# Kernel optimization log

Measured on AMD Instinct MI355X. Metric: run time of the kernel, lower is better.

The kernel has to match this reference:

```python
import jax, jax.numpy as jnp
import numpy as np


def _gru_cell(x, h, W_ih, W_hh, b_ih, b_hh):
    # PyTorch GRUCell math, gate order (r, z, n) along the 3*H axis.
    gi = x @ W_ih.T + b_ih          # [B, 3H]
    gh = h @ W_hh.T + b_hh          # [B, 3H]
    i_r, i_z, i_n = jnp.split(gi, 3, axis=-1)
    h_r, h_z, h_n = jnp.split(gh, 3, axis=-1)
    r = jax.nn.sigmoid(i_r + h_r)
    z = jax.nn.sigmoid(i_z + h_z)
    n = jnp.tanh(i_n + r * h_n)
    return (1.0 - z) * n + z * h


def setup_inputs() -> dict:
    key = jax.random.key(0)
    ks = jax.random.split(key, 12)
    V, E, H, L, B, T = 16000, 512, 1024, 2, 32, 64
    s = 0.05  # small init scale to keep gates unsaturated
    return {
        "hidden": jax.random.normal(ks[0], (L, B, H), jnp.float32),
        "embed": jax.random.normal(ks[1], (V, E), jnp.float32) * s,
        "W_ih0": jax.random.normal(ks[2], (3 * H, E), jnp.float32) * s,
        "W_hh0": jax.random.normal(ks[3], (3 * H, H), jnp.float32) * s,
        "b_ih0": jax.random.normal(ks[4], (3 * H,), jnp.float32) * s,
        "b_hh0": jax.random.normal(ks[5], (3 * H,), jnp.float32) * s,
        "W_ih1": jax.random.normal(ks[6], (3 * H, H), jnp.float32) * s,
        "W_hh1": jax.random.normal(ks[7], (3 * H, H), jnp.float32) * s,
        "b_ih1": jax.random.normal(ks[8], (3 * H,), jnp.float32) * s,
        "b_hh1": jax.random.normal(ks[9], (3 * H,), jnp.float32) * s,
        "W_out": jax.random.normal(ks[10], (V, H), jnp.float32) * s,
        "b_out": jax.random.normal(ks[11], (V,), jnp.float32) * s,
        "max_len": 64,
        "batch_size": 32,
    }


def reference(hidden, embed, W_ih0, W_hh0, b_ih0, b_hh0,
              W_ih1, W_hh1, b_ih1, b_hh1, W_out, b_out,
              max_len, batch_size):
    # target=None path: teacher_forcing_ratio forced to 0 -> greedy argmax decode.
    tok0 = jnp.zeros((batch_size,), jnp.int32)  # curr_token starts at zeros

    def step(carry, _):
        h, tok = carry                      # h: [2, B, H], tok: [B] int32
        x = embed[tok]                      # [B, E] embedding lookup
        h0 = _gru_cell(x, h[0], W_ih0, W_hh0, b_ih0, b_hh0)
        h1 = _gru_cell(h0, h[1], W_ih1, W_hh1, b_ih1, b_hh1)
        logits = h1 @ W_out.T + b_out       # [B, V]
        tok_next = jnp.argmax(logits, axis=1).astype(jnp.int32)
        return (jnp.stack([h0, h1]), tok_next), logits

    (_, _), outputs = jax.lax.scan(step, (hidden, tok0), None, length=max_len)
    return outputs  # [max_len, B, V]
```

## Files before the change

### kernel.cpp

```cpp
#include <hip/hip_runtime.h>
#include <stdint.h>

#define V_ 16000
#define E_ 512
#define H_ 1024
#define B_ 32
#define T_ 64
#define NG_ 3072
#define NR_ 6144
#define IHB_ 96

typedef float f32x4 __attribute__((ext_vector_type(4)));
typedef unsigned long long u64;

__device__ __forceinline__ unsigned int fkey(float f) {
    unsigned int u = __float_as_uint(f);
    return (u & 0x80000000u) ? ~u : (u | 0x80000000u);
}

__global__ void init_kernel(const float* __restrict__ hidden,
                            float* __restrict__ h0, float* __restrict__ h1,
                            u64* __restrict__ tokpk) {
    int idx = blockIdx.x * blockDim.x + threadIdx.x;
    if (idx < B_ * H_) {
        h0[idx] = hidden[idx];
        h1[idx] = hidden[B_ * H_ + idx];
    }
    if (idx < T_ * B_) tokpk[idx] = 0ull;
}

__device__ __forceinline__ void gemm_core(
    const float* wp0, const float* wp1,
    const float* ap0, const float* ap1,
    int nch, float* lds, int tid, float acc[4][4])
{
    const int k4s = tid & 15;
    const int r   = tid >> 4;
    const int dW0 = (r << 6) + ((k4s ^ (r & 7)) << 2);
    const int dW1 = dW0 + (16 << 6);
    const int ks   = tid >> 6;
    const int lane = tid & 63;
    const int vg = lane >> 3, bg = lane & 7;

    f32x4 tW0, tW1, tA0, tA1;
    tW0 = *(const f32x4*)(wp0 + (k4s << 2));
    tW1 = *(const f32x4*)(wp1 + (k4s << 2));
    tA0 = *(const f32x4*)(ap0 + (k4s << 2));
    tA1 = *(const f32x4*)(ap1 + (k4s << 2));
    *(f32x4*)&lds[dW0] = tW0;        *(f32x4*)&lds[dW1] = tW1;
    *(f32x4*)&lds[2048 + dW0] = tA0; *(f32x4*)&lds[2048 + dW1] = tA1;
    __syncthreads();

    int cur = 0;
    for (int c = 0; c < nch; c++) {
        if (c + 1 < nch) {
            const int nko = (c + 1) << 6;
            tW0 = *(const f32x4*)(wp0 + nko + (k4s << 2));
            tW1 = *(const f32x4*)(wp1 + nko + (k4s << 2));
            tA0 = *(const f32x4*)(ap0 + nko + (k4s << 2));
            tA1 = *(const f32x4*)(ap1 + nko + (k4s << 2));
        }
        const float* Wb = &lds[cur * 4096];
        const float* Ab = &lds[cur * 4096 + 2048];
        #pragma unroll
        for (int kk = 0; kk < 4; kk++) {
            const int k4 = ks * 4 + kk;
            f32x4 ww[4], ha[4];
            #pragma unroll
            for (int vi = 0; vi < 4; vi++)
                ww[vi] = *(const f32x4*)&Wb[((vg + 8*vi) << 6) + ((k4 ^ vg) << 2)];
            #pragma unroll
            for (int j = 0; j < 4; j++)
                ha[j] = *(const f32x4*)&Ab[((bg + 8*j) << 6) + ((k4 ^ bg) << 2)];
            #pragma unroll
            for (int vi = 0; vi < 4; vi++)
                #pragma unroll
                for (int j = 0; j < 4; j++)
                    acc[vi][j] += ww[vi].x*ha[j].x + ww[vi].y*ha[j].y
                                + ww[vi].z*ha[j].z + ww[vi].w*ha[j].w;
        }
        if (c + 1 < nch) {
            float* Wo = &lds[(cur ^ 1) * 4096];
            *(f32x4*)&Wo[dW0] = tW0;        *(f32x4*)&Wo[dW1] = tW1;
            *(f32x4*)&Wo[2048 + dW0] = tA0; *(f32x4*)&Wo[2048 + dW1] = tA1;
        }
        __syncthreads();
        cur ^= 1;
    }
}

__device__ __forceinline__ void ks_reduce(float* lds, int tid,
                                          float acc[4][4], float tv[16])
{
    const int ks = tid >> 6, lane = tid & 63;
    float* red = lds;
    float* dst = &red[(ks * 64 + lane) * 17];
    #pragma unroll
    for (int vi = 0; vi < 4; vi++)
        #pragma unroll
        for (int j = 0; j < 4; j++) dst[vi*4 + j] = acc[vi][j];
    __syncthreads();
    if (tid < 64) {
        #pragma unroll
        for (int c = 0; c < 16; c++) {
            float s = 0.f;
            #pragma unroll
            for (int k = 0; k < 4; k++) s += red[(k*64 + tid)*17 + c];
            tv[c] = s;
        }
    }
}

__global__ __launch_bounds__(256) void gemm_gru(
    const float* __restrict__ Wih, const float* __restrict__ Whh, int Kih,
    const float* __restrict__ xbase, int xld,
    const float* __restrict__ embed, const u64* __restrict__ tokprev,
    int t, int tmode,
    const float* __restrict__ hprev,
    float* __restrict__ gbuf)
{
    __shared__ float lds[8192];
    const int tid = threadIdx.x;
    const int blk = blockIdx.x;
    const int r = tid >> 4;

    const float *wp0, *wp1, *ap0, *ap1;
    int nch;
    if (blk < IHB_) {
        const int n0 = blk * 32;
        wp0 = Wih + (size_t)(n0 + r) * Kih;
        wp1 = Wih + (size_t)(n0 + r + 16) * Kih;
        if (tmode) {
            int tok0 = 0, tok1 = 0;
            if (t > 0) {
                tok0 = (int)(0xFFFFFFFFu - (unsigned)(tokprev[r] & 0xFFFFFFFFull));
                tok1 = (int)(0xFFFFFFFFu - (unsigned)(tokprev[r + 16] & 0xFFFFFFFFull));
            }
            ap0 = embed + (size_t)tok0 * Kih;
            ap1 = embed + (size_t)tok1 * Kih;
        } else {
            ap0 = xbase + (size_t)r * xld;
            ap1 = xbase + (size_t)(r + 16) * xld;
        }
        nch = Kih >> 6;
    } else {
        const int n0 = (blk - IHB_) * 32;
        wp0 = Whh + (size_t)(n0 + r) * H_;
        wp1 = Whh + (size_t)(n0 + r + 16) * H_;
        ap0 = hprev + (size_t)r * H_;
        ap1 = hprev + (size_t)(r + 16) * H_;
        nch = H_ >> 6;
    }

    float acc[4][4] = {};
    gemm_core(wp0, wp1, ap0, ap1, nch, lds, tid, acc);
    float tv[16];
    ks_reduce(lds, tid, acc, tv);
    if (tid < 64) {
        const int vgr = tid >> 3, bgr = tid & 7;
        const int nout0 = blk * 32;
        #pragma unroll
        for (int vi = 0; vi < 4; vi++)
            #pragma unroll
            for (int j = 0; j < 4; j++)
                gbuf[(size_t)(bgr + 8*j) * NR_ + nout0 + vgr + 8*vi] = tv[vi*4+j];
    }
}

__global__ __launch_bounds__(256) void combine_kernel(
    const float* __restrict__ gbuf,
    const float* __restrict__ bih, const float* __restrict__ bhh,
    const float* __restrict__ hprev, float* __restrict__ hnew)
{
    const int idx = blockIdx.x * 256 + threadIdx.x;
    const int b = idx >> 10, i = idx & 1023;
    const float* gb = gbuf + (size_t)b * NR_;
    const float gir = gb[i],        giz = gb[H_ + i],        gin = gb[2*H_ + i];
    const float ghr = gb[NG_ + i],  ghz = gb[NG_ + H_ + i],  ghn = gb[NG_ + 2*H_ + i];
    const float Sr = gir + ghr + bih[i] + bhh[i];
    const float Sz = giz + ghz + bih[H_ + i] + bhh[H_ + i];
    const float rr = 1.f / (1.f + expf(-Sr));
    const float zz = 1.f / (1.f + expf(-Sz));
    const float nn = tanhf(gin + bih[2*H_ + i] + rr * (ghn + bhh[2*H_ + i]));
    const float hp = hprev[(size_t)b * H_ + i];
    hnew[(size_t)b * H_ + i] = (1.f - zz) * nn + zz * hp;
}

__global__ __launch_bounds__(256) void logits_kernel(
    const float* __restrict__ h1, const float* __restrict__ Wout,
    const float* __restrict__ bout, float* __restrict__ out_t,
    u64* __restrict__ tokpk_t)
{
    __shared__ float lds[8192];
    const int tid = threadIdx.x;
    const int r = tid >> 4;
    const int v0 = blockIdx.x * 32;
    const float* wp0 = Wout + (size_t)(v0 + r) * H_;
    const float* wp1 = Wout + (size_t)(v0 + r + 16) * H_;
    const float* ap0 = h1 + (size_t)r * H_;
    const float* ap1 = h1 + (size_t)(r + 16) * H_;

    float acc[4][4] = {};
    gemm_core(wp0, wp1, ap0, ap1, H_ >> 6, lds, tid, acc);
    float tv[16];
    ks_reduce(lds, tid, acc, tv);

    float* totl = lds + 4*64*17;
    u64*   am   = (u64*)(lds + 4*64*17 + 32*33);
    if (tid < 64) {
        const int vgr = tid >> 3, bgr = tid & 7;
        #pragma unroll
        for (int vi = 0; vi < 4; vi++) {
            const float bo = bout[v0 + vgr + 8*vi];
            #pragma unroll
            for (int j = 0; j < 4; j++) tv[vi*4+j] += bo;
        }
        #pragma unroll
        for (int vi = 0; vi < 4; vi++)
            #pragma unroll
            for (int j = 0; j < 4; j++)
                totl[(bgr + 8*j) * 33 + vgr + 8*vi] = tv[vi*4+j];
        #pragma unroll
        for (int j = 0; j < 4; j++) {
            u64 best = 0ull;
            #pragma unroll
            for (int vi = 0; vi < 4; vi++) {
                const int v = v0 + vgr + 8*vi;
                u64 p = ((u64)fkey(tv[vi*4+j]) << 32)
                      | (u64)(0xFFFFFFFFu - (unsigned)v);
                best = p > best ? p : best;
            }
            am[(bgr + 8*j) * 8 + vgr] = best;
        }
    }
    __syncthreads();
    if (tid < 64) {
        const int b = tid >> 1, half = tid & 1;
        #pragma unroll
        for (int q = 0; q < 4; q++) {
            f32x4 o;
            o.x = totl[b*33 + half*16 + q*4 + 0];
            o.y = totl[b*33 + half*16 + q*4 + 1];
            o.z = totl[b*33 + half*16 + q*4 + 2];
            o.w = totl[b*33 + half*16 + q*4 + 3];
            __builtin_nontemporal_store(
                o, (f32x4*)(out_t + (size_t)b * V_ + v0 + half*16 + q*4));
        }
    }
    if (tid < 32) {
        u64 best = 0ull;
        #pragma unroll
        for (int q = 0; q < 8; q++) {
            u64 p = am[tid*8 + q];
            best = p > best ? p : best;
        }
        atomicMax(&tokpk_t[tid], best);
    }
}

extern "C" void kernel_launch(void* const* d_in, const int* in_sizes, int n_in,
                              void* d_out, int out_size, void* d_ws, size_t ws_size,
                              hipStream_t stream) {
    const float* hidden = (const float*)d_in[0];
    const float* embed  = (const float*)d_in[1];
    const float* Wih0   = (const float*)d_in[2];
    const float* Whh0   = (const float*)d_in[3];
    const float* bih0   = (const float*)d_in[4];
    const float* bhh0   = (const float*)d_in[5];
    const float* Wih1   = (const float*)d_in[6];
    const float* Whh1   = (const float*)d_in[7];
    const float* bih1   = (const float*)d_in[8];
    const float* bhh1   = (const float*)d_in[9];
    const float* Wout   = (const float*)d_in[10];
    const float* bout   = (const float*)d_in[11];
    float* out = (float*)d_out;

    const int BH = B_ * H_;
    float* ws = (float*)d_ws;
    float* h0buf = ws;
    float* h1buf = ws + 2 * BH;
    float* gbuf  = ws + 4 * BH;
    u64* tokpk = (u64*)(ws + 4 * BH + B_ * NR_);

    init_kernel<<<128, 256, 0, stream>>>(hidden, h0buf, h1buf, tokpk);

    for (int t = 0; t < T_; t++) {
        const int rp = t & 1, wpar = (t + 1) & 1;
        const u64* tokprev = tokpk + (size_t)(t > 0 ? t - 1 : 0) * B_;

        gemm_gru<<<NR_ / 32, 256, 0, stream>>>(
            Wih0, Whh0, E_, nullptr, 0, embed, tokprev, t, 1,
            h0buf + (size_t)rp * BH, gbuf);
        combine_kernel<<<128, 256, 0, stream>>>(
            gbuf, bih0, bhh0, h0buf + (size_t)rp * BH, h0buf + (size_t)wpar * BH);

        gemm_gru<<<NR_ / 32, 256, 0, stream>>>(
            Wih1, Whh1, H_, h0buf + (size_t)wpar * BH, H_, embed, tokprev, 0,
            0, h1buf + (size_t)rp * BH, gbuf);
        combine_kernel<<<128, 256, 0, stream>>>(
            gbuf, bih1, bhh1, h1buf + (size_t)rp * BH, h1buf + (size_t)wpar * BH);

        logits_kernel<<<V_ / 32, 256, 0, stream>>>(
            h1buf + (size_t)wpar * BH, Wout, bout,
            out + (size_t)t * B_ * V_, tokpk + (size_t)t * B_);
    }
}
```

Before: 4.374 ms.

## Fuse GRU gate GEMMs with combine step and shrink logits tiles

```diff
diff --git a/kernel.cpp b/kernel.cpp
--- a/kernel.cpp
+++ b/kernel.cpp
@@ -6,9 +6,6 @@
 #define H_ 1024
 #define B_ 32
 #define T_ 64
-#define NG_ 3072
-#define NR_ 6144
-#define IHB_ 96
 
 typedef float f32x4 __attribute__((ext_vector_type(4)));
 typedef unsigned long long u64;
@@ -29,161 +26,166 @@
     if (idx < T_ * B_) tokpk[idx] = 0ull;
 }
 
-__device__ __forceinline__ void gemm_core(
-    const float* wp0, const float* wp1,
-    const float* ap0, const float* ap1,
-    int nch, float* lds, int tid, float acc[4][4])
+__device__ __forceinline__ void gru_stream(
+    const float* const* sp, const int* dofs, int nch,
+    float* lds, int tid, float acc[3][2])
 {
-    const int k4s = tid & 15;
-    const int r   = tid >> 4;
-    const int dW0 = (r << 6) + ((k4s ^ (r & 7)) << 2);
-    const int dW1 = dW0 + (16 << 6);
-    const int ks   = tid >> 6;
-    const int lane = tid & 63;
-    const int vg = lane >> 3, bg = lane & 7;
-
-    f32x4 tW0, tW1, tA0, tA1;
-    tW0 = *(const f32x4*)(wp0 + (k4s << 2));
-    tW1 = *(const f32x4*)(wp1 + (k4s << 2));
-    tA0 = *(const f32x4*)(ap0 + (k4s << 2));
-    tA1 = *(const f32x4*)(ap1 + (k4s << 2));
-    *(f32x4*)&lds[dW0] = tW0;        *(f32x4*)&lds[dW1] = tW1;
-    *(f32x4*)&lds[2048 + dW0] = tA0; *(f32x4*)&lds[2048 + dW1] = tA1;
-    __syncthreads();
-
-    int cur = 0;
-    for (int c = 0; c < nch; c++) {
-        if (c + 1 < nch) {
-            const int nko = (c + 1) << 6;
-            tW0 = *(const f32x4*)(wp0 + nko + (k4s << 2));
-            tW1 = *(const f32x4*)(wp1 + nko + (k4s << 2));
-            tA0 = *(const f32x4*)(ap0 + nko + (k4s << 2));
-            tA1 = *(const f32x4*)(ap1 + nko + (k4s << 2));
-        }
-        const float* Wb = &lds[cur * 4096];
-        const float* Ab = &lds[cur * 4096 + 2048];
+    const int ks = tid >> 6, lane = tid & 63;
+    const int rg = lane >> 4, bgl = lane & 15;
+
+    auto compute = [&](const float* Wb) {
+        const float* Ab = Wb + 768;
         #pragma unroll
         for (int kk = 0; kk < 4; kk++) {
             const int k4 = ks * 4 + kk;
-            f32x4 ww[4], ha[4];
-            #pragma unroll
-            for (int vi = 0; vi < 4; vi++)
-                ww[vi] = *(const f32x4*)&Wb[((vg + 8*vi) << 6) + ((k4 ^ vg) << 2)];
-            #pragma unroll
-            for (int j = 0; j < 4; j++)
-                ha[j] = *(const f32x4*)&Ab[((bg + 8*j) << 6) + ((k4 ^ bg) << 2)];
-            #pragma unroll
-            for (int vi = 0; vi < 4; vi++)
+            f32x4 wv[3], av[2];
+            #pragma unroll
+            for (int vi = 0; vi < 3; vi++) {
+                const int row = vi * 4 + rg;
+                wv[vi] = *(const f32x4*)&Wb[row * 64 + ((k4 ^ (row & 7)) << 2)];
+            }
+            #pragma unroll
+            for (int j = 0; j < 2; j++) {
+                const int brow = bgl + 16 * j;
+                av[j] = *(const f32x4*)&Ab[brow * 64 + ((k4 ^ (brow & 7)) << 2)];
+            }
+            #pragma unroll
+            for (int vi = 0; vi < 3; vi++)
                 #pragma unroll
-                for (int j = 0; j < 4; j++)
-                    acc[vi][j] += ww[vi].x*ha[j].x + ww[vi].y*ha[j].y
-                                + ww[vi].z*ha[j].z + ww[vi].w*ha[j].w;
-        }
-        if (c + 1 < nch) {
-            float* Wo = &lds[(cur ^ 1) * 4096];
-            *(f32x4*)&Wo[dW0] = tW0;        *(f32x4*)&Wo[dW1] = tW1;
-            *(f32x4*)&Wo[2048 + dW0] = tA0; *(f32x4*)&Wo[2048 + dW1] = tA1;
-        }
+                for (int j = 0; j < 2; j++)
+                    acc[vi][j] += wv[vi].x*av[j].x + wv[vi].y*av[j].y
+                                + wv[vi].z*av[j].z + wv[vi].w*av[j].w;
+        }
+    };
+
+    f32x4 trA[3], trB[3];
+    #pragma unroll
+    for (int q = 0; q < 3; q++) trA[q] = *(const f32x4*)sp[q];
+    #pragma unroll
+    for (int q = 0; q < 3; q++) trB[q] = *(const f32x4*)(sp[q] + 64);
+    #pragma unroll
+    for (int q = 0; q < 3; q++) *(f32x4*)&lds[dofs[q]] = trA[q];
+    __syncthreads();
+
+    for (int c = 0; c < nch; c += 2) {
+        if (c + 2 < nch) {
+            #pragma unroll
+            for (int q = 0; q < 3; q++)
+                trA[q] = *(const f32x4*)(sp[q] + (c + 2) * 64);
+        }
+        compute(&lds[0]);
+        #pragma unroll
+        for (int q = 0; q < 3; q++) *(f32x4*)&lds[2816 + dofs[q]] = trB[q];
         __syncthreads();
-        cur ^= 1;
-    }
-}
-
-__device__ __forceinline__ void ks_reduce(float* lds, int tid,
-                                          float acc[4][4], float tv[16])
-{
-    const int ks = tid >> 6, lane = tid & 63;
-    float* red = lds;
-    float* dst = &red[(ks * 64 + lane) * 17];
-    #pragma unroll
-    for (int vi = 0; vi < 4; vi++)
-        #pragma unroll
-        for (int j = 0; j < 4; j++) dst[vi*4 + j] = acc[vi][j];
-    __syncthreads();
-    if (tid < 64) {
-        #pragma unroll
-        for (int c = 0; c < 16; c++) {
-            float s = 0.f;
-            #pragma unroll
-            for (int k = 0; k < 4; k++) s += red[(k*64 + tid)*17 + c];
-            tv[c] = s;
-        }
-    }
-}
-
-__global__ __launch_bounds__(256) void gemm_gru(
-    const float* __restrict__ Wih, const float* __restrict__ Whh, int Kih,
-    const float* __restrict__ xbase, int xld,
-    const float* __restrict__ embed, const u64* __restrict__ tokprev,
+        if (c + 3 < nch) {
+            #pragma unroll
+            for (int q = 0; q < 3; q++)
+                trB[q] = *(const f32x4*)(sp[q] + (c + 3) * 64);
+        }
+        compute(&lds[2816]);
+        if (c + 2 < nch) {
+            #pragma unroll
+            for (int q = 0; q < 3; q++) *(f32x4*)&lds[dofs[q]] = trA[q];
+        }
+        __syncthreads();
+    }
+}
+
+template<int KX>
+__global__ __launch_bounds__(256) void gru_fused(
+    const float* __restrict__ Wih, const float* __restrict__ Whh,
+    const float* __restrict__ xsrc, const u64* __restrict__ tokprev,
     int t, int tmode,
     const float* __restrict__ hprev,
-    float* __restrict__ gbuf)
+    const float* __restrict__ bih, const float* __restrict__ bhh,
+    float* __restrict__ hnew)
 {
-    __shared__ float lds[8192];
+    __shared__ float lds[5632];
     const int tid = threadIdx.x;
-    const int blk = blockIdx.x;
-    const int r = tid >> 4;
-
-    const float *wp0, *wp1, *ap0, *ap1;
-    int nch;
-    if (blk < IHB_) {
-        const int n0 = blk * 32;
-        wp0 = Wih + (size_t)(n0 + r) * Kih;
-        wp1 = Wih + (size_t)(n0 + r + 16) * Kih;
-        if (tmode) {
-            int tok0 = 0, tok1 = 0;
-            if (t > 0) {
-                tok0 = (int)(0xFFFFFFFFu - (unsigned)(tokprev[r] & 0xFFFFFFFFull));
-                tok1 = (int)(0xFFFFFFFFu - (unsigned)(tokprev[r + 16] & 0xFFFFFFFFull));
-            }
-            ap0 = embed + (size_t)tok0 * Kih;
-            ap1 = embed + (size_t)tok1 * Kih;
-        } else {
-            ap0 = xbase + (size_t)r * xld;
-            ap1 = xbase + (size_t)(r + 16) * xld;
-        }
-        nch = Kih >> 6;
-    } else {
-        const int n0 = (blk - IHB_) * 32;
-        wp0 = Whh + (size_t)(n0 + r) * H_;
-        wp1 = Whh + (size_t)(n0 + r + 16) * H_;
-        ap0 = hprev + (size_t)r * H_;
-        ap1 = hprev + (size_t)(r + 16) * H_;
-        nch = H_ >> 6;
-    }
-
-    float acc[4][4] = {};
-    gemm_core(wp0, wp1, ap0, ap1, nch, lds, tid, acc);
-    float tv[16];
-    ks_reduce(lds, tid, acc, tv);
-    if (tid < 64) {
-        const int vgr = tid >> 3, bgr = tid & 7;
-        const int nout0 = blk * 32;
-        #pragma unroll
-        for (int vi = 0; vi < 4; vi++)
-            #pragma unroll
-            for (int j = 0; j < 4; j++)
-                gbuf[(size_t)(bgr + 8*j) * NR_ + nout0 + vgr + 8*vi] = tv[vi*4+j];
-    }
-}
-
-__global__ __launch_bounds__(256) void combine_kernel(
-    const float* __restrict__ gbuf,
-    const float* __restrict__ bih, const float* __restrict__ bhh,
-    const float* __restrict__ hprev, float* __restrict__ hnew)
-{
-    const int idx = blockIdx.x * 256 + threadIdx.x;
-    const int b = idx >> 10, i = idx & 1023;
-    const float* gb = gbuf + (size_t)b * NR_;
-    const float gir = gb[i],        giz = gb[H_ + i],        gin = gb[2*H_ + i];
-    const float ghr = gb[NG_ + i],  ghz = gb[NG_ + H_ + i],  ghn = gb[NG_ + 2*H_ + i];
-    const float Sr = gir + ghr + bih[i] + bhh[i];
-    const float Sz = giz + ghz + bih[H_ + i] + bhh[H_ + i];
-    const float rr = 1.f / (1.f + expf(-Sr));
-    const float zz = 1.f / (1.f + expf(-Sz));
-    const float nn = tanhf(gin + bih[2*H_ + i] + rr * (ghn + bhh[2*H_ + i]));
-    const float hp = hprev[(size_t)b * H_ + i];
-    hnew[(size_t)b * H_ + i] = (1.f - zz) * nn + zz * hp;
+    const int i0 = blockIdx.x * 4;
+
+    float accI[3][2] = {}, accH[3][2] = {};
+
+    {
+        const float* sp[3]; int dofs[3];
+        #pragma unroll
+        for (int q = 0; q < 3; q++) {
+            int s = tid + q * 256; if (s >= 704) s = 0;
+            if (s < 192) {
+                const int row = s >> 4, k4 = s & 15;
+                sp[q] = Wih + (size_t)((row >> 2) * H_ + i0 + (row & 3)) * KX + k4 * 4;
+                dofs[q] = row * 64 + ((k4 ^ (row & 7)) << 2);
+            } else {
+                const int sa = s - 192, row = sa >> 4, k4 = sa & 15;
+                const float* ab;
+                if (tmode) {
+                    int tok = 0;
+                    if (t > 0)
+                        tok = (int)(0xFFFFFFFFu - (unsigned)(tokprev[row] & 0xFFFFFFFFull));
+                    ab = xsrc + (size_t)tok * KX;
+                } else {
+                    ab = xsrc + (size_t)row * KX;
+                }
+                sp[q] = ab + k4 * 4;
+                dofs[q] = 768 + row * 64 + ((k4 ^ (row & 7)) << 2);
+            }
+        }
+        gru_stream(sp, dofs, KX / 64, lds, tid, accI);
+    }
+    {
+        const float* sp[3]; int dofs[3];
+        #pragma unroll
+        for (int q = 0; q < 3; q++) {
+            int s = tid + q * 256; if (s >= 704) s = 0;
+            if (s < 192) {
+                const int row = s >> 4, k4 = s & 15;
+                sp[q] = Whh + (size_t)((row >> 2) * H_ + i0 + (row & 3)) * H_ + k4 * 4;
+                dofs[q] = row * 64 + ((k4 ^ (row & 7)) << 2);
+            } else {
+                const int sa = s - 192, row = sa >> 4, k4 = sa & 15;
+                sp[q] = hprev + (size_t)row * H_ + k4 * 4;
+                dofs[q] = 768 + row * 64 + ((k4 ^ (row & 7)) << 2);
+            }
+        }
+        gru_stream(sp, dofs, H_ / 64, lds, tid, accH);
+    }
+
+    {
+        const int ks = tid >> 6, lane = tid & 63;
+        float* dst = &lds[(ks * 64 + lane) * 13];
+        #pragma unroll
+        for (int vi = 0; vi < 3; vi++)
+            #pragma unroll
+            for (int j = 0; j < 2; j++) {
+                dst[vi * 2 + j]     = accI[vi][j];
+                dst[6 + vi * 2 + j] = accH[vi][j];
+            }
+    }
+    __syncthreads();
+    if (tid < 128) {
+        const int il = tid >> 5, b = tid & 31;
+        const int bgl = b & 15, j = b >> 4;
+        const int lsrc = il * 16 + bgl;
+        float sI[3], sH[3];
+        #pragma unroll
+        for (int vi = 0; vi < 3; vi++) {
+            float a = 0.f, h = 0.f;
+            #pragma unroll
+            for (int k = 0; k < 4; k++) {
+                a += lds[(k * 64 + lsrc) * 13 + vi * 2 + j];
+                h += lds[(k * 64 + lsrc) * 13 + 6 + vi * 2 + j];
+            }
+            sI[vi] = a; sH[vi] = h;
+        }
+        const int ii = i0 + il;
+        const float Sr = sI[0] + sH[0] + bih[ii] + bhh[ii];
+        const float Sz = sI[1] + sH[1] + bih[H_ + ii] + bhh[H_ + ii];
+        const float r = 1.f / (1.f + expf(-Sr));
+        const float z = 1.f / (1.f + expf(-Sz));
+        const float n = tanhf(sI[2] + bih[2 * H_ + ii] + r * (sH[2] + bhh[2 * H_ + ii]));
+        const float hp = hprev[(size_t)b * H_ + ii];
+        hnew[(size_t)b * H_ + ii] = (1.f - z) * n + z * hp;
+    }
 }
 
 __global__ __launch_bounds__(256) void logits_kernel(
@@ -191,67 +193,147 @@
     const float* __restrict__ bout, float* __restrict__ out_t,
     u64* __restrict__ tokpk_t)
 {
-    __shared__ float lds[8192];
+    __shared__ float lds[6144];
     const int tid = threadIdx.x;
-    const int r = tid >> 4;
-    const int v0 = blockIdx.x * 32;
-    const float* wp0 = Wout + (size_t)(v0 + r) * H_;
-    const float* wp1 = Wout + (size_t)(v0 + r + 16) * H_;
-    const float* ap0 = h1 + (size_t)r * H_;
-    const float* ap1 = h1 + (size_t)(r + 16) * H_;
-
-    float acc[4][4] = {};
-    gemm_core(wp0, wp1, ap0, ap1, H_ >> 6, lds, tid, acc);
-    float tv[16];
-    ks_reduce(lds, tid, acc, tv);
-
-    float* totl = lds + 4*64*17;
-    u64*   am   = (u64*)(lds + 4*64*17 + 32*33);
+    const int v0 = blockIdx.x * 16;
+    const int ks = tid >> 6, lane = tid & 63;
+    const int vg = lane >> 3, bg = lane & 7;
+
+    const float* sp[3]; int dofs[3];
+    #pragma unroll
+    for (int q = 0; q < 3; q++) {
+        const int s = tid + q * 256;
+        if (s < 256) {
+            const int row = s >> 4, k4 = s & 15;
+            sp[q] = Wout + (size_t)(v0 + row) * H_ + k4 * 4;
+            dofs[q] = row * 64 + ((k4 ^ (row & 7)) << 2);
+        } else {
+            const int sa = s - 256, row = sa >> 4, k4 = sa & 15;
+            sp[q] = h1 + (size_t)row * H_ + k4 * 4;
+            dofs[q] = 1024 + row * 64 + ((k4 ^ (row & 7)) << 2);
+        }
+    }
+
+    float acc[2][4] = {};
+    auto compute = [&](const float* Wb) {
+        const float* Ab = Wb + 1024;
+        #pragma unroll
+        for (int kk = 0; kk < 4; kk++) {
+            const int k4 = ks * 4 + kk;
+            f32x4 wv[2], av[4];
+            #pragma unroll
+            for (int vi = 0; vi < 2; vi++) {
+                const int row = vg + 8 * vi;
+                wv[vi] = *(const f32x4*)&Wb[row * 64 + ((k4 ^ (row & 7)) << 2)];
+            }
+            #pragma unroll
+            for (int j = 0; j < 4; j++) {
+                const int brow = bg + 8 * j;
+                av[j] = *(const f32x4*)&Ab[brow * 64 + ((k4 ^ (brow & 7)) << 2)];
+            }
+            #pragma unroll
+            for (int vi = 0; vi < 2; vi++)
+                #pragma unroll
+                for (int j = 0; j < 4; j++)
+                    acc[vi][j] += wv[vi].x*av[j].x + wv[vi].y*av[j].y
+                                + wv[vi].z*av[j].z + wv[vi].w*av[j].w;
+        }
+    };
+
+    f32x4 trA[3], trB[3];
+    #pragma unroll
+    for (int q = 0; q < 3; q++) trA[q] = *(const f32x4*)sp[q];
+    #pragma unroll
+    for (int q = 0; q < 3; q++) trB[q] = *(const f32x4*)(sp[q] + 64);
+    #pragma unroll
+    for (int q = 0; q < 3; q++) *(f32x4*)&lds[dofs[q]] = trA[q];
+    __syncthreads();
+
+    for (int c = 0; c < 16; c += 2) {
+        if (c + 2 < 16) {
+            #pragma unroll
+            for (int q = 0; q < 3; q++)
+                trA[q] = *(const f32x4*)(sp[q] + (c + 2) * 64);
+        }
+        compute(&lds[0]);
+        #pragma unroll
+        for (int q = 0; q < 3; q++) *(f32x4*)&lds[3072 + dofs[q]] = trB[q];
+        __syncthreads();
+        if (c + 3 < 16) {
+            #pragma unroll
+            for (int q = 0; q < 3; q++)
+                trB[q] = *(const f32x4*)(sp[q] + (c + 3) * 64);
+        }
+        compute(&lds[3072]);
+        if (c + 2 < 16) {
+            #pragma unroll
+            for (int q = 0; q < 3; q++) *(f32x4*)&lds[dofs[q]] = trA[q];
+        }
+        __syncthreads();
+    }
+
+    {
+        float* dst = &lds[(ks * 64 + lane) * 9];
+        #pragma unroll
+        for (int vi = 0; vi < 2; vi++)
+            #pragma unroll
+            for (int j = 0; j < 4; j++) dst[vi * 4 + j] = acc[vi][j];
+    }
+    __syncthreads();
+    float* totl = lds + 2304;
+    u64*   am   = (u64*)(lds + 2848);
     if (tid < 64) {
         const int vgr = tid >> 3, bgr = tid & 7;
-        #pragma unroll
-        for (int vi = 0; vi < 4; vi++) {
-            const float bo = bout[v0 + vgr + 8*vi];
-            #pragma unroll
-            for (int j = 0; j < 4; j++) tv[vi*4+j] += bo;
-        }
-        #pragma unroll
-        for (int vi = 0; vi < 4; vi++)
+        float tv[2][4];
+        #pragma unroll
+        for (int vi = 0; vi < 2; vi++) {
+            const float bo = bout[v0 + vgr + 8 * vi];
+            #pragma unroll
+            for (int j = 0; j < 4; j++) {
+                float s = 0.f;
+                #pragma unroll
+                for (int k = 0; k < 4; k++)
+                    s += lds[(k * 64 + vgr * 8 + bgr) * 9 + vi * 4 + j];
+                tv[vi][j] = s + bo;
+            }
+        }
+        #pragma unroll
+        for (int vi = 0; vi < 2; vi++)
             #pragma unroll
             for (int j = 0; j < 4; j++)
-                totl[(bgr + 8*j) * 33 + vgr + 8*vi] = tv[vi*4+j];
+                totl[(bgr + 8 * j) * 17 + vgr + 8 * vi] = tv[vi][j];
         #pragma unroll
         for (int j = 0; j < 4; j++) {
             u64 best = 0ull;
             #pragma unroll
-            for (int vi = 0; vi < 4; vi++) {
-                const int v = v0 + vgr + 8*vi;
-                u64 p = ((u64)fkey(tv[vi*4+j]) << 32)
+            for (int vi = 0; vi < 2; vi++) {
+                const int v = v0 + vgr + 8 * vi;
+                u64 p = ((u64)fkey(tv[vi][j]) << 32)
                       | (u64)(0xFFFFFFFFu - (unsigned)v);
                 best = p > best ? p : best;
             }
-            am[(bgr + 8*j) * 8 + vgr] = best;
+            am[(bgr + 8 * j) * 8 + vgr] = best;
         }
     }
     __syncthreads();
     if (tid < 64) {
         const int b = tid >> 1, half = tid & 1;
         #pragma unroll
-        for (int q = 0; q < 4; q++) {
+        for (int q = 0; q < 2; q++) {
             f32x4 o;
-            o.x = totl[b*33 + half*16 + q*4 + 0];
-            o.y = totl[b*33 + half*16 + q*4 + 1];
-            o.z = totl[b*33 + half*16 + q*4 + 2];
-            o.w = totl[b*33 + half*16 + q*4 + 3];
+            o.x = totl[b * 17 + half * 8 + q * 4 + 0];
+            o.y = totl[b * 17 + half * 8 + q * 4 + 1];
+            o.z = totl[b * 17 + half * 8 + q * 4 + 2];
+            o.w = totl[b * 17 + half * 8 + q * 4 + 3];
             __builtin_nontemporal_store(
-                o, (f32x4*)(out_t + (size_t)b * V_ + v0 + half*16 + q*4));
+                o, (f32x4*)(out_t + (size_t)b * V_ + v0 + half * 8 + q * 4));
         }
     }
     if (tid < 32) {
         u64 best = 0ull;
         #pragma unroll
         for (int q = 0; q < 8; q++) {
-            u64 p = am[tid*8 + q];
+            u64 p = am[tid * 8 + q];
             best = p > best ? p : best;
         }
         atomicMax(&tokpk_t[tid], best);
@@ -279,29 +361,24 @@
     float* ws = (float*)d_ws;
     float* h0buf = ws;
     float* h1buf = ws + 2 * BH;
-    float* gbuf  = ws + 4 * BH;
-    u64* tokpk = (u64*)(ws + 4 * BH + B_ * NR_);
+    u64* tokpk = (u64*)(ws + 4 * BH);
 
     init_kernel<<<128, 256, 0, stream>>>(hidden, h0buf, h1buf, tokpk);
 
     for (int t = 0; t < T_; t++) {
-        const int rp = t & 1, wpar = (t + 1) & 1;
+        const int rp = t & 1, wp = (t + 1) & 1;
         const u64* tokprev = tokpk + (size_t)(t > 0 ? t - 1 : 0) * B_;
 
-        gemm_gru<<<NR_ / 32, 256, 0, stream>>>(
-            Wih0, Whh0, E_, nullptr, 0, embed, tokprev, t, 1,
-            h0buf + (size_t)rp * BH, gbuf);
-        combine_kernel<<<128, 256, 0, stream>>>(
-            gbuf, bih0, bhh0, h0buf + (size_t)rp * BH, h0buf + (size_t)wpar * BH);
-
-        gemm_gru<<<NR_ / 32, 256, 0, stream>>>(
-            Wih1, Whh1, H_, h0buf + (size_t)wpar * BH, H_, embed, tokprev, 0,
-            0, h1buf + (size_t)rp * BH, gbuf);
-        combine_kernel<<<128, 256, 0, stream>>>(
-            gbuf, bih1, bhh1, h1buf + (size_t)rp * BH, h1buf + (size_t)wpar * BH);
-
-        logits_kernel<<<V_ / 32, 256, 0, stream>>>(
-            h1buf + (size_t)wpar * BH, Wout, bout,
+        gru_fused<E_><<<H_ / 4, 256, 0, stream>>>(
+            Wih0, Whh0, embed, tokprev, t, 1,
+            h0buf + (size_t)rp * BH, bih0, bhh0, h0buf + (size_t)wp * BH);
+
+        gru_fused<H_><<<H_ / 4, 256, 0, stream>>>(
+            Wih1, Whh1, h0buf + (size_t)wp * BH, nullptr, 0, 0,
+            h1buf + (size_t)rp * BH, bih1, bhh1, h1buf + (size_t)wp * BH);
+
+        logits_kernel<<<V_ / 16, 256, 0, stream>>>(
+            h1buf + (size_t)wp * BH, Wout, bout,
             out + (size_t)t * B_ * V_, tokpk + (size_t)t * B_);
     }
 }
```

Result: slower. 8.099 ms (+85.2%).

## Rewrite logits kernel with async global-to-LDS double buffering and smaller tiles

Applied to the files above, without the earlier changes.

```diff
diff --git a/kernel.cpp b/kernel.cpp
--- a/kernel.cpp
+++ b/kernel.cpp
@@ -16,6 +16,12 @@
 __device__ __forceinline__ unsigned int fkey(float f) {
     unsigned int u = __float_as_uint(f);
     return (u & 0x80000000u) ? ~u : (u | 0x80000000u);
+}
+
+__device__ __forceinline__ void gload_lds16(const float* g, float* l) {
+    __builtin_amdgcn_global_load_lds(
+        (const __attribute__((address_space(1))) void*)g,
+        (__attribute__((address_space(3))) void*)l, 16, 0, 0);
 }
 
 __global__ void init_kernel(const float* __restrict__ hidden,
@@ -191,67 +197,118 @@
     const float* __restrict__ bout, float* __restrict__ out_t,
     u64* __restrict__ tokpk_t)
 {
-    __shared__ float lds[8192];
-    const int tid = threadIdx.x;
-    const int r = tid >> 4;
-    const int v0 = blockIdx.x * 32;
-    const float* wp0 = Wout + (size_t)(v0 + r) * H_;
-    const float* wp1 = Wout + (size_t)(v0 + r + 16) * H_;
-    const float* ap0 = h1 + (size_t)r * H_;
-    const float* ap1 = h1 + (size_t)(r + 16) * H_;
-
-    float acc[4][4] = {};
-    gemm_core(wp0, wp1, ap0, ap1, H_ >> 6, lds, tid, acc);
-    float tv[16];
-    ks_reduce(lds, tid, acc, tv);
-
-    float* totl = lds + 4*64*17;
-    u64*   am   = (u64*)(lds + 4*64*17 + 32*33);
+    __shared__ float lds[3360];
+    const int tid  = threadIdx.x;
+    const int lane = tid & 63;
+    const int wave = tid >> 6;
+    const int v0   = blockIdx.x * 16;
+    const int vg = lane >> 3, bg = lane & 7;
+
+    const int srow = 4 * wave + (lane >> 4);
+    const int sk4  = (lane & 15) ^ (srow & 7);
+    const float* gsrc = Wout + (size_t)(v0 + srow) * H_ + sk4 * 4;
+    float* ldst0 = &lds[wave * 256];
+    float* ldst1 = &lds[1024 + wave * 256];
+
+    const float* ap[4];
+    #pragma unroll
+    for (int j = 0; j < 4; j++) ap[j] = h1 + (size_t)(bg + 8*j) * H_;
+
+    float acc[2][4] = {};
+
+    gload_lds16(gsrc, ldst0);
+    __syncthreads();
+
+    int cur = 0;
+    for (int c = 0; c < 16; c++) {
+        if (c + 1 < 16)
+            gload_lds16(gsrc + (c + 1) * 64, cur ? ldst0 : ldst1);
+        const float* Wb = &lds[cur * 1024];
+        #pragma unroll
+        for (int kk = 0; kk < 4; kk++) {
+            const int k4 = wave * 4 + kk;
+            f32x4 wv[2], av[4];
+            #pragma unroll
+            for (int vi = 0; vi < 2; vi++) {
+                const int row = vg + 8 * vi;
+                wv[vi] = *(const f32x4*)&Wb[(row << 6) + ((k4 ^ (row & 7)) << 2)];
+            }
+            #pragma unroll
+            for (int j = 0; j < 4; j++)
+                av[j] = *(const f32x4*)(ap[j] + c * 64 + k4 * 4);
+            #pragma unroll
+            for (int vi = 0; vi < 2; vi++)
+                #pragma unroll
+                for (int j = 0; j < 4; j++)
+                    acc[vi][j] += wv[vi].x*av[j].x + wv[vi].y*av[j].y
+                                + wv[vi].z*av[j].z + wv[vi].w*av[j].w;
+        }
+        __syncthreads();
+        cur ^= 1;
+    }
+
+    {
+        float* dst = &lds[(wave * 64 + lane) * 9];
+        #pragma unroll
+        for (int vi = 0; vi < 2; vi++)
+            #pragma unroll
+            for (int j = 0; j < 4; j++) dst[vi * 4 + j] = acc[vi][j];
+    }
+    __syncthreads();
+    float* totl = lds + 2304;
+    u64*   am   = (u64*)(lds + 2848);
     if (tid < 64) {
         const int vgr = tid >> 3, bgr = tid & 7;
-        #pragma unroll
-        for (int vi = 0; vi < 4; vi++) {
-            const float bo = bout[v0 + vgr + 8*vi];
-            #pragma unroll
-            for (int j = 0; j < 4; j++) tv[vi*4+j] += bo;
-        }
-        #pragma unroll
-        for (int vi = 0; vi < 4; vi++)
+        float tv[2][4];
+        #pragma unroll
+        for (int vi = 0; vi < 2; vi++) {
+            const float bo = bout[v0 + vgr + 8 * vi];
+            #pragma unroll
+            for (int j = 0; j < 4; j++) {
+                float s = 0.f;
+                #pragma unroll
+                for (int k = 0; k < 4; k++)
+                    s += lds[(k * 64 + vgr * 8 + bgr) * 9 + vi * 4 + j];
+                tv[vi][j] = s + bo;
+            }
+        }
+        #pragma unroll
+        for (int vi = 0; vi < 2; vi++)
             #pragma unroll
             for (int j = 0; j < 4; j++)
-                totl[(bgr + 8*j) * 33 + vgr + 8*vi] = tv[vi*4+j];
+                totl[(bgr + 8 * j) * 17 + vgr + 8 * vi] = tv[vi][j];
         #pragma unroll
         for (int j = 0; j < 4; j++) {
             u64 best = 0ull;
             #pragma unroll
-            for (int vi = 0; vi < 4; vi++) {
-                const int v = v0 + vgr + 8*vi;
-                u64 p = ((u64)fkey(tv[vi*4+j]) << 32)
+            for (int vi = 0; vi < 2; vi++) {
+                const int v = v0 + vgr + 8 * vi;
+                u64 p = ((u64)fkey(tv[vi][j]) << 32)
                       | (u64)(0xFFFFFFFFu - (unsigned)v);
                 best = p > best ? p : best;
             }
-            am[(bgr + 8*j) * 8 + vgr] = best;
+            am[(bgr + 8 * j) * 8 + vgr] = best;
         }
     }
     __syncthreads();
     if (tid < 64) {
         const int b = tid >> 1, half = tid & 1;
         #pragma unroll
-        for (int q = 0; q < 4; q++) {
+        for (int q = 0; q < 2; q++) {
             f32x4 o;
-            o.x = totl[b*33 + half*16 + q*4 + 0];
-            o.y = totl[b*33 + half*16 + q*4 + 1];
-            o.z = totl[b*33 + half*16 + q*4 + 2];
-            o.w = totl[b*33 + half*16 + q*4 + 3];
+            o.x = totl[b * 17 + half * 8 + q * 4 + 0];
+            o.y = totl[b * 17 + half * 8 + q * 4 + 1];
+            o.z = totl[b * 17 + half * 8 + q * 4 + 2];
+            o.w = totl[b * 17 + half * 8 + q * 4 + 3];
             __builtin_nontemporal_store(
-                o, (f32x4*)(out_t + (size_t)b * V_ + v0 + half*16 + q*4));
+                o, (f32x4*)(out_t + (size_t)b * V_ + v0 + half * 8 + q * 4));
         }
     }
     if (tid < 32) {
         u64 best = 0ull;
         #pragma unroll
         for (int q = 0; q < 8; q++) {
-            u64 p = am[tid*8 + q];
+            u64 p = am[tid * 8 + q];
             best = p > best ? p : best;
         }
         atomicMax(&tokpk_t[tid], best);
@@ -285,23 +342,23 @@
     init_kernel<<<128, 256, 0, stream>>>(hidden, h0buf, h1buf, tokpk);
 
     for (int t = 0; t < T_; t++) {
-        const int rp = t & 1, wpar = (t + 1) & 1;
+        const int rp = t & 1, wp = (t + 1) & 1;
         const u64* tokprev = tokpk + (size_t)(t > 0 ? t - 1 : 0) * B_;
 
         gemm_gru<<<NR_ / 32, 256, 0, stream>>>(
             Wih0, Whh0, E_, nullptr, 0, embed, tokprev, t, 1,
             h0buf + (size_t)rp * BH, gbuf);
         combine_kernel<<<128, 256, 0, stream>>>(
-            gbuf, bih0, bhh0, h0buf + (size_t)rp * BH, h0buf + (size_t)wpar * BH);
+            gbuf, bih0, bhh0, h0buf + (size_t)rp * BH, h0buf + (size_t)wp * BH);
 
         gemm_gru<<<NR_ / 32, 256, 0, stream>>>(
-            Wih1, Whh1, H_, h0buf + (size_t)wpar * BH, H_, embed, tokprev, 0,
+            Wih1, Whh1, H_, h0buf + (size_t)wp * BH, H_, embed, tokprev, 0,
             0, h1buf + (size_t)rp * BH, gbuf);
         combine_kernel<<<128, 256, 0, stream>>>(
-            gbuf, bih1, bhh1, h1buf + (size_t)rp * BH, h1buf + (size_t)wpar * BH);
-
-        logits_kernel<<<V_ / 32, 256, 0, stream>>>(
-            h1buf + (size_t)wpar * BH, Wout, bout,
+            gbuf, bih1, bhh1, h1buf + (size_t)rp * BH, h1buf + (size_t)wp * BH);
+
+        logits_kernel<<<V_ / 16, 256, 0, stream>>>(
+            h1buf + (size_t)wp * BH, Wout, bout,
             out + (size_t)t * B_ * V_, tokpk + (size_t)t * B_);
     }
 }
```

After: 10.38 ms. 2.37x slower.
